# Kernel tuning notes

Hardware: AMD Instinct MI355X
Metric: run time of the kernel (lower is better)

Reference implementation:

```python
import jax, jax.numpy as jnp
import numpy as np

BS, IN_CH, HID, N_NODES, STEPS = 8, 1, 64, 1024, 64


def setup_inputs() -> dict:
    key = jax.random.key(0)
    ks = jax.random.split(key, 13)
    s = 1.0 / np.sqrt(HID).astype(np.float32)
    x = jax.random.normal(ks[0], (BS, IN_CH, N_NODES, STEPS), jnp.float32)
    mask = jax.random.randint(ks[1], (BS, IN_CH, N_NODES, STEPS), 0, 2) > 0
    # scale graphs so the 64-step diffusion recurrence is contractive
    graph = jax.random.uniform(ks[2], (N_NODES, N_NODES), jnp.float32) / N_NODES
    ind_graph = jax.random.uniform(ks[3], (N_NODES, N_NODES), jnp.float32) / N_NODES
    # learned initial state h0: (hidden, n_nodes), N(0, 1/sqrt(hidden))
    h0 = jax.random.normal(ks[4], (HID, N_NODES), jnp.float32) * s
    # Conv1d(k=1) heads: weight (out_ch, in_ch) + bias (out_ch,)
    W_init = jax.random.normal(ks[5], (IN_CH, HID), jnp.float32) * s
    b_init = jax.random.normal(ks[6], (IN_CH,), jnp.float32) * s
    W_out = jax.random.normal(ks[7], (IN_CH, HID), jnp.float32) * s
    b_out = jax.random.normal(ks[8], (IN_CH,), jnp.float32) * s
    # GRUCell (single layer): gates stacked [r, z, n] along first axis
    W_ih = jax.random.normal(ks[9], (3 * HID, IN_CH), jnp.float32) * s
    W_hh = jax.random.normal(ks[10], (3 * HID, HID), jnp.float32) * s
    b_ih = jax.random.normal(ks[11], (3 * HID,), jnp.float32) * s
    b_hh = jax.random.normal(ks[12], (3 * HID,), jnp.float32) * s
    return {"x": x, "mask": mask, "graph": graph, "ind_graph": ind_graph,
            "h0": h0, "W_init": W_init, "b_init": b_init,
            "W_out": W_out, "b_out": b_out,
            "W_ih": W_ih, "W_hh": W_hh, "b_ih": b_ih, "b_hh": b_hh}


def _frame_forward(x, mask, graph, ind_graph, h0, W_init, b_init,
                   W_out, b_out, W_ih, W_hh, b_ih, b_hh):
    bs = x.shape[0]
    h_init = jnp.broadcast_to(h0[None], (bs, HID, N_NODES))

    def step(h, inp):
        x_now, m_now = inp                                  # (bs, in_ch, V), (bs, in_ch, V)
        x_hat1 = jnp.einsum('bhv,oh->bov', h, W_init) + b_init[None, :, None]
        x_hat = jnp.where(m_now, x_now, x_hat1)
        h_diff = jnp.einsum('bhv,wv->bhw', h, graph)        # graph diffusion of state
        x_g = jnp.einsum('bcv,wv->bcw', x_hat, ind_graph)   # graph diffusion of input
        # GRUCell, vectorized over all nodes at once
        gi = jnp.einsum('bcv,gc->bgv', x_g, W_ih) + b_ih[None, :, None]
        gh = jnp.einsum('bhv,gh->bgv', h_diff, W_hh) + b_hh[None, :, None]
        ir, iz, inn = jnp.split(gi, 3, axis=1)
        hr, hz, hn = jnp.split(gh, 3, axis=1)
        r = jax.nn.sigmoid(ir + hr)
        z = jax.nn.sigmoid(iz + hz)
        n = jnp.tanh(inn + r * hn)
        h_new = (1.0 - z) * n + z * h_diff                  # (bs, hid, V)
        x_hat2 = jnp.einsum('bhv,oh->bov', h_new, W_out) + b_out[None, :, None]
        return h_new, (x_hat2, x_hat1, h_new)

    xs = (jnp.moveaxis(x, -1, 0), jnp.moveaxis(mask, -1, 0))  # steps leading
    _, (imps, preds, reprs) = jax.lax.scan(step, h_init, xs)
    imps = jnp.moveaxis(imps, 0, -1)    # (bs, in_ch, V, steps)
    preds = jnp.moveaxis(preds, 0, -1)  # (bs, in_ch, V, steps)
    reprs = jnp.moveaxis(reprs, 0, -1)  # (bs, hid, V, steps)
    return imps, preds, reprs


def reference(x, mask, graph, ind_graph, h0, W_init, b_init,
              W_out, b_out, W_ih, W_hh, b_ih, b_hh):
    return _frame_forward(x, mask, graph, ind_graph, h0, W_init, b_init,
                          W_out, b_out, W_ih, W_hh, b_ih, b_hh)
```

## Files before the change

kernel.cpp:

```cpp
#include <hip/hip_runtime.h>
#include <hip/hip_bf16.h>

#define BS 8
#define HID 64
#define NV 1024
#define NSTEP 64
#define HSTRIDE (BS*HID*NV)

#define IMPS_OFF  0
#define PREDS_OFF 524288
#define REPRS_OFF 1048576

typedef unsigned short u16;
typedef __attribute__((ext_vector_type(8))) short bf8;
typedef __attribute__((ext_vector_type(4))) float f4;
typedef __attribute__((ext_vector_type(4))) unsigned int u32x4;

__device__ int g_bar[128];

__device__ __forceinline__ u16 f2bf(float f){
    __hip_bfloat16 h = __float2bfloat16(f);
    return *reinterpret_cast<u16*>(&h);
}
__device__ __forceinline__ bf8 ld8bf(const float* src){
    float v[8];
    *(float4*)&v[0] = *(const float4*)src;
    *(float4*)&v[4] = *(const float4*)(src + 4);
    union { u16 u[8]; bf8 b; } r;
    #pragma unroll
    for (int j = 0; j < 8; ++j) r.u[j] = f2bf(v[j]);
    return r.b;
}

__device__ __forceinline__ bf8 ldcc(const u16* p){
    bf8 r;
    asm volatile("global_load_dwordx4 %0, %1, off sc0 sc1" : "=v"(r) : "v"(p));
    return r;
}
__device__ __forceinline__ f4 ldccf4(const float* p){
    f4 r;
    asm volatile("global_load_dwordx4 %0, %1, off sc0 sc1" : "=v"(r) : "v"(p));
    return r;
}
__device__ __forceinline__ void stcc16(u16* p, u32x4 v){
    asm volatile("global_store_dwordx4 %0, %1, off sc0 sc1" :: "v"(p), "v"(v) : "memory");
}
__device__ __forceinline__ void stccf(float* p, float v){
    asm volatile("global_store_dword %0, %1, off sc0 sc1" :: "v"(p), "v"(v) : "memory");
}
__device__ __forceinline__ void waitvm0(){
    asm volatile("s_waitcnt vmcnt(0)" ::: "memory");
    __builtin_amdgcn_sched_barrier(0);
}

__global__ void conv_k(const float* __restrict__ h0, u16* __restrict__ hws){
    int f = blockIdx.x * blockDim.x + threadIdx.x;
    int l   = f & 63;
    int sel = (f >> 6) & 1;
    int k   = (f >> 7) & 31;
    int hh  = (f >> 12) & 1;
    int row = hh*32 + sel*16 + (l & 15);
    int col = k*32 + (l >> 4)*8;
    bf8 p = ld8bf(h0 + (size_t)row*NV + col);
    *(bf8*)(hws + (size_t)f*8) = p;
}

__global__ void frag_k(const float* __restrict__ g, u16* __restrict__ gff){
    int f = blockIdx.x * blockDim.x + threadIdx.x;
    int l    = f & 63;
    int k    = (f >> 6) & 31;
    int wt   = (f >> 11) & 1;
    int tile = f >> 12;
    int row = tile*32 + wt*16 + (l & 15);
    int col = k*32 + (l >> 4)*8;
    bf8 p = ld8bf(g + (size_t)row*NV + col);
    *(bf8*)(gff + (size_t)f*8) = p;
}

__global__ void prep_k(const float* __restrict__ x, const int* __restrict__ mask,
                       float* __restrict__ xmt){
    __shared__ float tx[64][65];
    __shared__ int   tm[64][65];
    int b  = blockIdx.x >> 4;
    int v0 = (blockIdx.x & 15) << 6;
    int tid = threadIdx.x;
    int q = tid >> 6, l = tid & 63;
    #pragma unroll 4
    for (int r = 0; r < 16; ++r){
        int vv = r*4 + q;
        size_t idx = ((size_t)b*NV + v0 + vv)*64 + l;
        tx[vv][l] = x[idx];
        tm[vv][l] = mask[idx];
    }
    __syncthreads();
    #pragma unroll 4
    for (int r = 0; r < 16; ++r){
        int tt = r*4 + q;
        float xv = tx[l][tt];
        xmt[((size_t)b*NSTEP + tt)*NV + v0 + l] = tm[l][tt] ? xv : __builtin_inff();
    }
}

__global__ void init_k(const float* __restrict__ h0, const float* __restrict__ Wini,
                       const float* __restrict__ bini, float* __restrict__ out,
                       float* __restrict__ predsT){
    if (blockIdx.x == 0 && threadIdx.x < 128) g_bar[threadIdx.x] = 0;
    int v = blockIdx.x * blockDim.x + threadIdx.x;
    if (v < NV){
        float s = 0.f;
        for (int h = 0; h < HID; ++h) s += h0[h*NV + v] * Wini[h];
        s += bini[0];
        for (int b = 0; b < BS; ++b){
            out[PREDS_OFF + (size_t)b*65536 + (size_t)v*64] = s;
            predsT[(size_t)b*NSTEP*NV + v] = s;
        }
    }
}

__global__ __launch_bounds__(256, 1) void persist_k(
    u16* __restrict__ hws,
    const u16* __restrict__ gff, const float* __restrict__ ig,
    const float* __restrict__ Whh,
    const float* __restrict__ xmt, float* __restrict__ predsT,
    const float* __restrict__ Wih, const float* __restrict__ bih,
    const float* __restrict__ bhh,
    const float* __restrict__ Wini, const float* __restrict__ bini,
    const float* __restrict__ Wo, const float* __restrict__ bo,
    float* out, float* __restrict__ rtmp, int staged)
{
    __shared__ float xh_s[NV];
    __shared__ __align__(16) u16 hdb[32][72];
    __shared__ __align__(16) float hnf[32][68];
    __shared__ float xg_s[32];
    __shared__ float r1[8][33], r2[8][33];

    const int tid  = threadIdx.x;
    const int b    = blockIdx.x >> 5;
    const int tile = blockIdx.x & 31;
    const int w0   = tile << 5;
    const int lane = tid & 63;
    const int wv   = tid >> 6;
    const int wt   = wv & 1;
    const int hh   = wv >> 1;
    const int m16  = lane & 15;
    const int q    = lane >> 4;

    bf8 wf[3][2][2];
    #pragma unroll
    for (int gi = 0; gi < 3; ++gi)
        #pragma unroll
        for (int ht = 0; ht < 2; ++ht)
            #pragma unroll
            for (int ks = 0; ks < 2; ++ks)
                wf[gi][ht][ks] = ld8bf(Whh
                    + (size_t)(gi*64 + hh*32 + ht*16 + m16)*64 + ks*32 + q*8);

    const u16* gB = gff + ((size_t)(tile*2 + wt)*32)*512 + lane*8;
    const int v4 = tid * 4;
    int* const cb = g_bar + (b << 4);

    #pragma unroll 1
    for (int t = 0; t < NSTEP; ++t){
        const u16* hin  = hws + (size_t)(t & 1) * HSTRIDE;
        u16*       hout = hws + (size_t)((t+1) & 1) * HSTRIDE;

        float4 xm = *(const float4*)(xmt + ((size_t)b*NSTEP + t)*NV + v4);
        f4 pv = ldccf4(predsT + ((size_t)b*NSTEP + t)*NV + v4);

        const u16* hA = hin + (size_t)b*65536 + (size_t)hh*32768 + lane*8;
        f4 accA0 = {0.f,0.f,0.f,0.f}, accA1 = {0.f,0.f,0.f,0.f};
        #pragma unroll 1
        for (int g = 0; g < 8; ++g){
            const u16* gk = gB + (size_t)g*2048;
            bf8 g0 = *(const bf8*)(gk);
            bf8 g1 = *(const bf8*)(gk + 512);
            bf8 g2 = *(const bf8*)(gk + 1024);
            bf8 g3 = *(const bf8*)(gk + 1536);
            const u16* hk = hA + (size_t)g*4096;
            bf8 a00 = ldcc(hk);
            bf8 a10 = ldcc(hk + 512);
            bf8 a01 = ldcc(hk + 1024);
            bf8 a11 = ldcc(hk + 1536);
            bf8 a02 = ldcc(hk + 2048);
            bf8 a12 = ldcc(hk + 2560);
            bf8 a03 = ldcc(hk + 3072);
            bf8 a13 = ldcc(hk + 3584);
            waitvm0();
            accA0 = __builtin_amdgcn_mfma_f32_16x16x32_bf16(a00, g0, accA0, 0, 0, 0);
            accA1 = __builtin_amdgcn_mfma_f32_16x16x32_bf16(a10, g0, accA1, 0, 0, 0);
            accA0 = __builtin_amdgcn_mfma_f32_16x16x32_bf16(a01, g1, accA0, 0, 0, 0);
            accA1 = __builtin_amdgcn_mfma_f32_16x16x32_bf16(a11, g1, accA1, 0, 0, 0);
            accA0 = __builtin_amdgcn_mfma_f32_16x16x32_bf16(a02, g2, accA0, 0, 0, 0);
            accA1 = __builtin_amdgcn_mfma_f32_16x16x32_bf16(a12, g2, accA1, 0, 0, 0);
            accA0 = __builtin_amdgcn_mfma_f32_16x16x32_bf16(a03, g3, accA0, 0, 0, 0);
            accA1 = __builtin_amdgcn_mfma_f32_16x16x32_bf16(a13, g3, accA1, 0, 0, 0);
        }

        waitvm0();
        {
            float4 xh;
            xh.x = (__float_as_uint(xm.x) == 0x7f800000u) ? pv.x : xm.x;
            xh.y = (__float_as_uint(xm.y) == 0x7f800000u) ? pv.y : xm.y;
            xh.z = (__float_as_uint(xm.z) == 0x7f800000u) ? pv.z : xm.z;
            xh.w = (__float_as_uint(xm.w) == 0x7f800000u) ? pv.w : xm.w;
            *(float4*)&xh_s[v4] = xh;
        }
        #pragma unroll
        for (int ht = 0; ht < 2; ++ht){
            f4 a = ht ? accA1 : accA0;
            ushort4 pk;
            pk.x = f2bf(a[0]); pk.y = f2bf(a[1]); pk.z = f2bf(a[2]); pk.w = f2bf(a[3]);
            *(ushort4*)&hdb[wt*16 + m16][hh*32 + ht*16 + q*4] = pk;
        }
        __syncthreads();

        {
            int w = tid >> 3, p = tid & 7;
            const float* igr = ig + (size_t)(w0 + w)*NV + p*8;
            float acc = 0.f;
            #pragma unroll
            for (int k = 0; k < 16; ++k){
                float4 ga = *(const float4*)(igr + k*64);
                float4 gc = *(const float4*)(igr + k*64 + 4);
                const float* xv = &xh_s[p*8 + k*64];
                acc += ga.x*xv[0] + ga.y*xv[1] + ga.z*xv[2] + ga.w*xv[3]
                     + gc.x*xv[4] + gc.y*xv[5] + gc.z*xv[6] + gc.w*xv[7];
            }
            acc += __shfl_xor(acc, 1);
            acc += __shfl_xor(acc, 2);
            acc += __shfl_xor(acc, 4);
            if (p == 0) xg_s[w] = acc;
        }

        f4 accG[3][2];
        #pragma unroll
        for (int i = 0; i < 3; ++i){ accG[i][0] = (f4){0,0,0,0}; accG[i][1] = (f4){0,0,0,0}; }
        #pragma unroll
        for (int ks = 0; ks < 2; ++ks){
            bf8 bfr = *(const bf8*)&hdb[wt*16 + m16][ks*32 + q*8];
            #pragma unroll
            for (int gi = 0; gi < 3; ++gi){
                #pragma unroll
                for (int ht = 0; ht < 2; ++ht){
                    accG[gi][ht] = __builtin_amdgcn_mfma_f32_16x16x32_bf16(
                        wf[gi][ht][ks], bfr, accG[gi][ht], 0, 0, 0);
                }
            }
        }
        __syncthreads();

        {
            int wme = wt*16 + m16;
            float xg = xg_s[wme];
            #pragma unroll
            for (int ht = 0; ht < 2; ++ht){
                f4 hd4 = ht ? accA1 : accA0;
                f4 hn4;
                int hb4 = hh*32 + ht*16 + q*4;
                #pragma unroll
                for (int r = 0; r < 4; ++r){
                    int h = hb4 + r;
                    float ir  = xg * Wih[h]       + bih[h];
                    float iz  = xg * Wih[64 + h]  + bih[64 + h];
                    float inn = xg * Wih[128 + h] + bih[128 + h];
                    float hr  = accG[0][ht][r] + bhh[h];
                    float hz  = accG[1][ht][r] + bhh[64 + h];
                    float hnn = accG[2][ht][r] + bhh[128 + h];
                    float rg = 1.f / (1.f + __expf(-(ir + hr)));
                    float zg = 1.f / (1.f + __expf(-(iz + hz)));
                    float ng = tanhf(inn + rg * hnn);
                    hn4[r] = (1.f - zg) * ng + zg * hd4[r];
                }
                *(f4*)&hnf[wme][hb4] = hn4;
            }
        }
        __syncthreads();

        {
            int w2 = tid & 31, hg = tid >> 5;
            float s1 = 0.f, s2 = 0.f;
            #pragma unroll
            for (int j = 0; j < 8; ++j){
                float hv = hnf[w2][hg*8 + j];
                s1 += Wini[hg*8 + j] * hv;
                s2 += Wo[hg*8 + j]   * hv;
            }
            r1[hg][w2] = s1; r2[hg][w2] = s2;
        }
        {
            int h = tid >> 2, wq = tid & 3;
            float vals[8];
            #pragma unroll
            for (int j = 0; j < 8; ++j) vals[j] = hnf[wq*8 + j][h];
            union { u16 pk[8]; u32x4 v; } u;
            #pragma unroll
            for (int j = 0; j < 8; ++j) u.pk[j] = f2bf(vals[j]);
            size_t ho = (size_t)b*65536
                      + ((size_t)((h >> 5)*32 + tile)*2 + ((h >> 4) & 1))*512
                      + wq*128 + (h & 15)*8;
            stcc16(hout + ho, u.v);
            if (staged){
                float* rp = rtmp + (((size_t)t*BS + b)*HID + h)*NV + w0 + wq*8;
                float4 a = {vals[0], vals[1], vals[2], vals[3]};
                float4 c = {vals[4], vals[5], vals[6], vals[7]};
                *(float4*)rp       = a;
                *(float4*)(rp + 4) = c;
            } else {
                size_t rb = REPRS_OFF + (((size_t)b*HID + h)*NV + w0 + wq*8)*64 + t;
                #pragma unroll
                for (int j = 0; j < 8; ++j) out[rb + (size_t)j*64] = vals[j];
            }
        }
        __syncthreads();
        if (tid < 32){
            int w = tid, wg = w0 + w;
            float s1 = 0.f, s2 = 0.f;
            #pragma unroll
            for (int hg = 0; hg < 8; ++hg){ s1 += r1[hg][w]; s2 += r2[hg][w]; }
            s1 += bini[0]; s2 += bo[0];
            size_t base = (size_t)b*65536 + (size_t)wg*64;
            out[IMPS_OFF + base + t] = s2;
            if (t < NSTEP - 1){
                out[PREDS_OFF + base + t + 1] = s1;
                stccf(predsT + ((size_t)b*NSTEP + t + 1)*NV + wg, s1);
            }
        }

        if (t < NSTEP - 1){
            waitvm0();
            __syncthreads();
            if (tid == 0){
                __hip_atomic_fetch_add(cb, 1, __ATOMIC_RELAXED, __HIP_MEMORY_SCOPE_AGENT);
                int target = 32 * (t + 1);
                while (__hip_atomic_load(cb, __ATOMIC_RELAXED, __HIP_MEMORY_SCOPE_AGENT) < target)
                    __builtin_amdgcn_s_sleep(2);
            }
            __syncthreads();
        }
    }
}

__global__ void transpose_k(const float* __restrict__ rtmp, float* __restrict__ out){
    __shared__ float tile[64][65];
    int bh = blockIdx.x >> 4;
    int b  = bh >> 6, h = bh & 63;
    int v0 = (blockIdx.x & 15) << 6;
    int tid = threadIdx.x;
    int q = tid >> 6, l = tid & 63;
    #pragma unroll 4
    for (int r = 0; r < 16; ++r){
        int tt = r*4 + q;
        tile[tt][l] = rtmp[(((size_t)tt*BS + b)*HID + h)*NV + v0 + l];
    }
    __syncthreads();
    #pragma unroll 4
    for (int r = 0; r < 16; ++r){
        int vv = r*4 + q;
        out[REPRS_OFF + (((size_t)b*HID + h)*NV + v0 + vv)*64 + l] = tile[l][vv];
    }
}

extern "C" void kernel_launch(void* const* d_in, const int* in_sizes, int n_in,
                              void* d_out, int out_size, void* d_ws, size_t ws_size,
                              hipStream_t stream) {
    const float* x     = (const float*)d_in[0];
    const int*   mask  = (const int*)  d_in[1];
    const float* graph = (const float*)d_in[2];
    const float* ind   = (const float*)d_in[3];
    const float* h0    = (const float*)d_in[4];
    const float* Wini  = (const float*)d_in[5];
    const float* bini  = (const float*)d_in[6];
    const float* Wo    = (const float*)d_in[7];
    const float* bo    = (const float*)d_in[8];
    const float* Wih   = (const float*)d_in[9];
    const float* Whh   = (const float*)d_in[10];
    const float* bih   = (const float*)d_in[11];
    const float* bhh   = (const float*)d_in[12];
    float* out = (float*)d_out;

    char* ws = (char*)d_ws;
    u16*   hws    = (u16*)(ws);
    u16*   gff    = (u16*)(ws + ((size_t)2<<20));
    float* xmt    = (float*)(ws + ((size_t)4<<20));
    float* predsT = (float*)(ws + ((size_t)6<<20));
    float* rtmp   = (float*)(ws + ((size_t)8<<20));
    size_t need_staged = ((size_t)8<<20) + (size_t)NSTEP*BS*HID*NV*4;
    int staged = (ws_size >= need_staged) ? 1 : 0;

    conv_k<<<dim3(256), dim3(256), 0, stream>>>(h0, hws);
    frag_k<<<dim3(512), dim3(256), 0, stream>>>(graph, gff);
    prep_k<<<dim3(128), dim3(256), 0, stream>>>(x, mask, xmt);
    init_k<<<dim3(4), dim3(256), 0, stream>>>(h0, Wini, bini, out, predsT);

    persist_k<<<dim3(256), dim3(256), 0, stream>>>(
        hws, gff, ind, Whh, xmt, predsT,
        Wih, bih, bhh, Wini, bini, Wo, bo, out, rtmp, staged);

    if (staged) transpose_k<<<dim3(8192), dim3(256), 0, stream>>>(rtmp, out);
}
```

Before: 905.6 us.

## Replace atomic-counter barrier with per-block flags and software-pipeline MFMA loads

```diff
diff --git a/kernel.cpp b/kernel.cpp
--- a/kernel.cpp
+++ b/kernel.cpp
@@ -16,7 +16,7 @@
 typedef __attribute__((ext_vector_type(4))) float f4;
 typedef __attribute__((ext_vector_type(4))) unsigned int u32x4;
 
-__device__ int g_bar[128];
+__device__ int g_flag[4096];
 
 __device__ __forceinline__ u16 f2bf(float f){
     __hip_bfloat16 h = __float2bfloat16(f);
@@ -37,15 +37,33 @@
     asm volatile("global_load_dwordx4 %0, %1, off sc0 sc1" : "=v"(r) : "v"(p));
     return r;
 }
+__device__ __forceinline__ bf8 ldg16(const u16* p){
+    bf8 r;
+    asm volatile("global_load_dwordx4 %0, %1, off" : "=v"(r) : "v"(p));
+    return r;
+}
 __device__ __forceinline__ f4 ldccf4(const float* p){
     f4 r;
     asm volatile("global_load_dwordx4 %0, %1, off sc0 sc1" : "=v"(r) : "v"(p));
     return r;
 }
+__device__ __forceinline__ f4 ldgf4(const float* p){
+    f4 r;
+    asm volatile("global_load_dwordx4 %0, %1, off" : "=v"(r) : "v"(p));
+    return r;
+}
 __device__ __forceinline__ void stcc16(u16* p, u32x4 v){
     asm volatile("global_store_dwordx4 %0, %1, off sc0 sc1" :: "v"(p), "v"(v) : "memory");
 }
 __device__ __forceinline__ void stccf(float* p, float v){
+    asm volatile("global_store_dword %0, %1, off sc0 sc1" :: "v"(p), "v"(v) : "memory");
+}
+__device__ __forceinline__ int ldci(const int* p){
+    int r;
+    asm volatile("global_load_dword %0, %1, off sc0 sc1" : "=v"(r) : "v"(p));
+    return r;
+}
+__device__ __forceinline__ void stci(int* p, int v){
     asm volatile("global_store_dword %0, %1, off sc0 sc1" :: "v"(p), "v"(v) : "memory");
 }
 __device__ __forceinline__ void waitvm0(){
@@ -104,8 +122,9 @@
 __global__ void init_k(const float* __restrict__ h0, const float* __restrict__ Wini,
                        const float* __restrict__ bini, float* __restrict__ out,
                        float* __restrict__ predsT){
-    if (blockIdx.x == 0 && threadIdx.x < 128) g_bar[threadIdx.x] = 0;
-    int v = blockIdx.x * blockDim.x + threadIdx.x;
+    int gid = blockIdx.x * blockDim.x + threadIdx.x;
+    for (int i = gid; i < 4096; i += 1024) g_flag[i] = 0;
+    int v = gid;
     if (v < NV){
         float s = 0.f;
         for (int h = 0; h < HID; ++h) s += h0[h*NV + v] * Wini[h];
@@ -157,46 +176,47 @@
 
     const u16* gB = gff + ((size_t)(tile*2 + wt)*32)*512 + lane*8;
     const int v4 = tid * 4;
-    int* const cb = g_bar + (b << 4);
 
     #pragma unroll 1
     for (int t = 0; t < NSTEP; ++t){
         const u16* hin  = hws + (size_t)(t & 1) * HSTRIDE;
         u16*       hout = hws + (size_t)((t+1) & 1) * HSTRIDE;
 
-        float4 xm = *(const float4*)(xmt + ((size_t)b*NSTEP + t)*NV + v4);
+        f4 xm = ldgf4(xmt + ((size_t)b*NSTEP + t)*NV + v4);
         f4 pv = ldccf4(predsT + ((size_t)b*NSTEP + t)*NV + v4);
 
         const u16* hA = hin + (size_t)b*65536 + (size_t)hh*32768 + lane*8;
+        bf8 Ga[3][4], Aa[3][4], Ab[3][4];
         f4 accA0 = {0.f,0.f,0.f,0.f}, accA1 = {0.f,0.f,0.f,0.f};
-        #pragma unroll 1
-        for (int g = 0; g < 8; ++g){
-            const u16* gk = gB + (size_t)g*2048;
-            bf8 g0 = *(const bf8*)(gk);
-            bf8 g1 = *(const bf8*)(gk + 512);
-            bf8 g2 = *(const bf8*)(gk + 1024);
-            bf8 g3 = *(const bf8*)(gk + 1536);
-            const u16* hk = hA + (size_t)g*4096;
-            bf8 a00 = ldcc(hk);
-            bf8 a10 = ldcc(hk + 512);
-            bf8 a01 = ldcc(hk + 1024);
-            bf8 a11 = ldcc(hk + 1536);
-            bf8 a02 = ldcc(hk + 2048);
-            bf8 a12 = ldcc(hk + 2560);
-            bf8 a03 = ldcc(hk + 3072);
-            bf8 a13 = ldcc(hk + 3584);
-            waitvm0();
-            accA0 = __builtin_amdgcn_mfma_f32_16x16x32_bf16(a00, g0, accA0, 0, 0, 0);
-            accA1 = __builtin_amdgcn_mfma_f32_16x16x32_bf16(a10, g0, accA1, 0, 0, 0);
-            accA0 = __builtin_amdgcn_mfma_f32_16x16x32_bf16(a01, g1, accA0, 0, 0, 0);
-            accA1 = __builtin_amdgcn_mfma_f32_16x16x32_bf16(a11, g1, accA1, 0, 0, 0);
-            accA0 = __builtin_amdgcn_mfma_f32_16x16x32_bf16(a02, g2, accA0, 0, 0, 0);
-            accA1 = __builtin_amdgcn_mfma_f32_16x16x32_bf16(a12, g2, accA1, 0, 0, 0);
-            accA0 = __builtin_amdgcn_mfma_f32_16x16x32_bf16(a03, g3, accA0, 0, 0, 0);
-            accA1 = __builtin_amdgcn_mfma_f32_16x16x32_bf16(a13, g3, accA1, 0, 0, 0);
-        }
-
-        waitvm0();
+        #define LOADCH(c, bk) { \
+            _Pragma("unroll") \
+            for (int j = 0; j < 4; ++j){ \
+                int kk = (c)*4 + j; \
+                Ga[bk][j] = ldg16(gB + kk*512); \
+                Aa[bk][j] = ldcc(hA + kk*1024); \
+                Ab[bk][j] = ldcc(hA + kk*1024 + 512); \
+            } }
+        LOADCH(0, 0)
+        LOADCH(1, 1)
+        #pragma unroll
+        for (int c = 0; c < 8; ++c){
+            if (c < 6){
+                LOADCH(c + 2, (c + 2) % 3)
+                asm volatile("s_waitcnt vmcnt(24)" ::: "memory");
+            } else if (c == 6){
+                asm volatile("s_waitcnt vmcnt(12)" ::: "memory");
+            } else {
+                asm volatile("s_waitcnt vmcnt(0)" ::: "memory");
+            }
+            __builtin_amdgcn_sched_barrier(0);
+            #pragma unroll
+            for (int j = 0; j < 4; ++j){
+                accA0 = __builtin_amdgcn_mfma_f32_16x16x32_bf16(Aa[c % 3][j], Ga[c % 3][j], accA0, 0, 0, 0);
+                accA1 = __builtin_amdgcn_mfma_f32_16x16x32_bf16(Ab[c % 3][j], Ga[c % 3][j], accA1, 0, 0, 0);
+            }
+        }
+        #undef LOADCH
+
         {
             float4 xh;
             xh.x = (__float_as_uint(xm.x) == 0x7f800000u) ? pv.x : xm.x;
@@ -329,11 +349,15 @@
         if (t < NSTEP - 1){
             waitvm0();
             __syncthreads();
-            if (tid == 0){
-                __hip_atomic_fetch_add(cb, 1, __ATOMIC_RELAXED, __HIP_MEMORY_SCOPE_AGENT);
-                int target = 32 * (t + 1);
-                while (__hip_atomic_load(cb, __ATOMIC_RELAXED, __HIP_MEMORY_SCOPE_AGENT) < target)
-                    __builtin_amdgcn_s_sleep(2);
+            if (tid == 0) stci(g_flag + (blockIdx.x << 4), t + 1);
+            if (wv == 0){
+                const int* fp = g_flag + (((b << 5) + (lane & 31)) << 4);
+                while (true){
+                    int f = ldci(fp);
+                    asm volatile("s_waitcnt vmcnt(0)" ::: "memory");
+                    if (__all(f >= t + 1)) break;
+                    __builtin_amdgcn_s_sleep(1);
+                }
             }
             __syncthreads();
         }
```

Result: no change. 909.0 us (+0.4%).
